# Performance work log

Measured on AMD Instinct MI355X. Metric: run time of the kernel, lower is better.

The kernel has to match this reference:

```python
import jax, jax.numpy as jnp
import numpy as np

B, S, H = 2, 1024, 1024
NH, NKV, HD = 16, 4, 64
F = 2816
E, K = 8, 2
WIN = 256
EPS = 1e-5
THETA = 10000.0


def setup_inputs() -> dict:
    key = jax.random.key(0)
    ks = jax.random.split(key, 13)
    n = lambda k, shp, s=0.02: jax.random.normal(k, shp, jnp.float32) * s
    return dict(
        hidden_states=jax.random.normal(ks[0], (B, S, H), jnp.float32),
        ln1_w=jnp.ones((H,), jnp.float32),
        q_w=n(ks[1], (H, NH * HD)),
        k_w=n(ks[2], (H, NKV * HD)),
        v_w=n(ks[3], (H, NKV * HD)),
        o_w=n(ks[4], (NH * HD, H)),
        res_ln_w=jnp.ones((H,), jnp.float32),
        rw1=n(ks[5], (H, H)),
        rw3=n(ks[6], (H, H)),
        rw2=n(ks[7], (H, H)),
        post_ln_w=jnp.ones((H,), jnp.float32),
        gate_w=n(ks[8], (H, E)),
        e_w1=n(ks[9], (E, H, F)),
        e_w3=n(ks[10], (E, H, F)),
        e_w2=n(ks[11], (E, F, H)),
    )


def _rms(x, w):
    v = jnp.mean(jnp.square(x), -1, keepdims=True)
    return x * jax.lax.rsqrt(v + EPS) * w


def _rope(x):
    # x: [B,S,h,HD]; standard rotate-half RoPE
    pos = jnp.arange(S, dtype=jnp.float32)
    inv = 1.0 / (THETA ** (jnp.arange(0, HD, 2, dtype=jnp.float32) / HD))
    ang = pos[:, None] * inv  # [S, HD/2]
    cos = jnp.concatenate([jnp.cos(ang)] * 2, -1)[None, :, None, :]
    sin = jnp.concatenate([jnp.sin(ang)] * 2, -1)[None, :, None, :]
    x1, x2 = jnp.split(x, 2, axis=-1)
    rot = jnp.concatenate([-x2, x1], -1)
    return x * cos + rot * sin


def _attn(x, q_w, k_w, v_w, o_w):
    q = (x @ q_w).reshape(B, S, NH, HD)
    k = (x @ k_w).reshape(B, S, NKV, HD)
    v = (x @ v_w).reshape(B, S, NKV, HD)
    q, k = _rope(q), _rope(k)
    rep = NH // NKV
    k = jnp.repeat(k, rep, axis=2)
    v = jnp.repeat(v, rep, axis=2)
    sc = jnp.einsum('bqhd,bkhd->bhqk', q, k) * (HD ** -0.5)
    qi = jnp.arange(S)[:, None]
    ki = jnp.arange(S)[None, :]
    mask = (ki <= qi) & (qi - ki < WIN)  # causal sliding window
    sc = jnp.where(mask[None, None], sc, jnp.finfo(sc.dtype).min)
    p = jax.nn.softmax(sc, -1)
    o = jnp.einsum('bhqk,bkhd->bqhd', p, v).reshape(B, S, NH * HD)
    return o @ o_w


def _mlp(x, w1, w3, w2):
    return (jax.nn.silu(x @ w1) * (x @ w3)) @ w2


def _moe(x, gate_w, w1, w3, w2):
    xf = x.reshape(-1, H)  # [T,H]
    T = xf.shape[0]
    logits = xf @ gate_w
    probs = jax.nn.softmax(logits.astype(jnp.float32), -1)
    tw, ti = jax.lax.top_k(probs, K)
    tw = tw / jnp.sum(tw, -1, keepdims=True)
    # combine weights [T,E] via scatter of top-k weights
    cw = jnp.zeros((T, E), jnp.float32).at[jnp.arange(T)[:, None], ti].add(tw)
    h = jax.nn.silu(jnp.einsum('th,ehf->etf', xf, w1)) * jnp.einsum('th,ehf->etf', xf, w3)
    y = jnp.einsum('etf,efh->eth', h, w2)
    out = jnp.einsum('te,eth->th', cw, y)
    return out.reshape(B, S, H)


def reference(hidden_states, ln1_w, q_w, k_w, v_w, o_w, res_ln_w, rw1, rw3, rw2,
              post_ln_w, gate_w, e_w1, e_w3, e_w2):
    residual_input = hidden_states
    h = _rms(hidden_states, ln1_w)
    h = _attn(h, q_w, k_w, v_w, o_w)
    residual_attn = residual_input + h
    # parallel residual dense MLP path (is_residual_mlp=True -> ffn_dim=hidden)
    h = _rms(residual_attn, res_ln_w)
    h = _mlp(h, rw1, rw3, rw2)
    residual_residual = residual_attn + h
    # sparse MoE path operates on the ORIGINAL layer input (Arctic parallel path)
    h = _rms(residual_input, post_ln_w)
    h = _moe(h, gate_w, e_w1, e_w3, e_w2)
    return residual_residual + h
```

## Files before the change

### kernel.cpp

```cpp
#include <hip/hip_runtime.h>
#include <hip/hip_bf16.h>
#include <math.h>

#define B_    2
#define S_    1024
#define H_    1024
#define NH_   16
#define NKV_  4
#define HD_   64
#define F_    2816
#define E_    8
#define WIN_  256
#define T_    (B_*S_)
#define EPS_  1e-5f
#define QKVN_ 1536

typedef __hip_bfloat16 bf16;
using f32x4  = __attribute__((ext_vector_type(4))) float;
using bf16x8 = __attribute__((ext_vector_type(8))) short;

__device__ __forceinline__ float silu_f(float x) { return x / (1.0f + expf(-x)); }

__device__ __forceinline__ unsigned short f2bf(float v) {
  __hip_bfloat16 b = __float2bfloat16(v);
  return *reinterpret_cast<unsigned short*>(&b);
}

__device__ __forceinline__ void stage16(const void* g, void* l) {
#if defined(__has_builtin) && __has_builtin(__builtin_amdgcn_global_load_lds)
  __builtin_amdgcn_global_load_lds((const __attribute__((address_space(1))) unsigned int*)g,
                                   (__attribute__((address_space(3))) unsigned int*)l,
                                   16, 0, 0);
#else
  *(float4*)l = *(const float4*)g;
#endif
}

__global__ void rope_table_kernel(float* __restrict__ costab, float* __restrict__ sintab,
                                  int* __restrict__ counts) {
  int idx = blockIdx.x * blockDim.x + threadIdx.x;
  if (blockIdx.x == 0 && threadIdx.x < E_) counts[threadIdx.x] = 0;
  if (idx >= S_ * 32) return;
  int s = idx >> 5, j = idx & 31;
  float inv = powf(10000.0f, -(float)j / 32.0f);
  float ang = (float)s * inv;
  costab[idx] = cosf(ang);
  sintab[idx] = sinf(ang);
}

__global__ void transpose_cvt_kernel(const float* __restrict__ src, bf16* __restrict__ dst,
                                     int K, int N) {
  __shared__ float tile[32][33];
  const size_t bstride = (size_t)K * N;
  src += bstride * blockIdx.z;
  dst += bstride * blockIdx.z;
  int bk = blockIdx.x * 32, bn = blockIdx.y * 32;
  int tx = threadIdx.x & 31, ty = threadIdx.x >> 5;
  #pragma unroll
  for (int i = 0; i < 4; ++i)
    tile[ty + i * 8][tx] = src[(size_t)(bk + ty + i * 8) * N + bn + tx];
  __syncthreads();
  #pragma unroll
  for (int i = 0; i < 4; ++i)
    dst[(size_t)(bn + ty + i * 8) * K + bk + tx] = __float2bfloat16(tile[tx][ty + i * 8]);
}

struct TransBatch { const float* src[5]; bf16* dst[5]; };
__global__ void transpose_cvt5_kernel(TransBatch tb, int K, int N) {
  __shared__ float tile[32][33];
  const float* src = tb.src[blockIdx.z];
  bf16* dst = tb.dst[blockIdx.z];
  int bk = blockIdx.x * 32, bn = blockIdx.y * 32;
  int tx = threadIdx.x & 31, ty = threadIdx.x >> 5;
  #pragma unroll
  for (int i = 0; i < 4; ++i)
    tile[ty + i * 8][tx] = src[(size_t)(bk + ty + i * 8) * N + bn + tx];
  __syncthreads();
  #pragma unroll
  for (int i = 0; i < 4; ++i)
    dst[(size_t)(bn + ty + i * 8) * K + bk + tx] = __float2bfloat16(tile[tx][ty + i * 8]);
}

__global__ void rms_kernel(const float* __restrict__ x, const float* __restrict__ w,
                           bf16* __restrict__ ob) {
  const int row = blockIdx.x, t = threadIdx.x;
  const float* xr = x + (size_t)row * H_;
  float4 v = *(const float4*)(&xr[t * 4]);
  float ss = v.x*v.x + v.y*v.y + v.z*v.z + v.w*v.w;
  #pragma unroll
  for (int o = 32; o > 0; o >>= 1) ss += __shfl_xor(ss, o);
  __shared__ float red[4];
  if ((t & 63) == 0) red[t >> 6] = ss;
  __syncthreads();
  float tot = red[0] + red[1] + red[2] + red[3];
  float scale = rsqrtf(tot * (1.0f / H_) + EPS_);
  float4 wv = *(const float4*)(&w[t * 4]);
  ushort4 pk = { f2bf(v.x*scale*wv.x), f2bf(v.y*scale*wv.y),
                 f2bf(v.z*scale*wv.z), f2bf(v.w*scale*wv.w) };
  *(ushort4*)((unsigned short*)ob + (size_t)row * H_ + t * 4) = pk;
}

__global__ void rms_gate_kernel(const float* __restrict__ x, const float* __restrict__ w,
                                const float* __restrict__ gw, bf16* __restrict__ ob,
                                int* __restrict__ counts, int* __restrict__ entries,
                                float* __restrict__ wgt) {
  const int row = blockIdx.x, t = threadIdx.x;
  const float* xr = x + (size_t)row * H_;
  float4 v = *(const float4*)(&xr[t * 4]);
  float ss = v.x*v.x + v.y*v.y + v.z*v.z + v.w*v.w;
  #pragma unroll
  for (int o = 32; o > 0; o >>= 1) ss += __shfl_xor(ss, o);
  __shared__ float red[4];
  __shared__ float sm[4][8];
  if ((t & 63) == 0) red[t >> 6] = ss;
  __syncthreads();
  float tot = red[0] + red[1] + red[2] + red[3];
  float scale = rsqrtf(tot * (1.0f / H_) + EPS_);
  float4 wv = *(const float4*)(&w[t * 4]);
  float o0 = v.x*scale*wv.x, o1 = v.y*scale*wv.y, o2 = v.z*scale*wv.z, o3 = v.w*scale*wv.w;
  ushort4 pk = { f2bf(o0), f2bf(o1), f2bf(o2), f2bf(o3) };
  *(ushort4*)((unsigned short*)ob + (size_t)row * H_ + t * 4) = pk;
  const float* gr = gw + (size_t)(t * 4) * E_;
  float acc[E_];
  #pragma unroll
  for (int e = 0; e < E_; ++e)
    acc[e] = o0 * gr[e] + o1 * gr[E_ + e] + o2 * gr[2 * E_ + e] + o3 * gr[3 * E_ + e];
  #pragma unroll
  for (int e = 0; e < E_; ++e) {
    #pragma unroll
    for (int o = 32; o > 0; o >>= 1) acc[e] += __shfl_xor(acc[e], o);
  }
  if ((t & 63) == 0) {
    #pragma unroll
    for (int e = 0; e < E_; ++e) sm[t >> 6][e] = acc[e];
  }
  __syncthreads();
  if (t == 0) {
    float lg[E_];
    #pragma unroll
    for (int e = 0; e < E_; ++e) lg[e] = sm[0][e] + sm[1][e] + sm[2][e] + sm[3][e];
    float m = lg[0];
    #pragma unroll
    for (int e = 1; e < E_; ++e) m = fmaxf(m, lg[e]);
    float p[E_];
    #pragma unroll
    for (int e = 0; e < E_; ++e) p[e] = expf(lg[e] - m);
    int i0 = 0; float b0 = p[0];
    #pragma unroll
    for (int e = 1; e < E_; ++e) if (p[e] > b0) { b0 = p[e]; i0 = e; }
    int i1 = -1; float b1 = -1.f;
    #pragma unroll
    for (int e = 0; e < E_; ++e) if (e != i0 && p[e] > b1) { b1 = p[e]; i1 = e; }
    float inv = 1.f / (b0 + b1);
    wgt[row * 2 + 0] = b0 * inv;
    wgt[row * 2 + 1] = b1 * inv;
    int pos0 = atomicAdd(&counts[i0], 1);
    entries[i0 * T_ + pos0] = row * 2 + 0;
    int pos1 = atomicAdd(&counts[i1], 1);
    entries[i1 * T_ + pos1] = row * 2 + 1;
  }
}

template <int BN, bool ADD_RES>
__global__ __launch_bounds__(256)
void mm_kernel(const bf16* __restrict__ A, const bf16* __restrict__ Bt,
               const float* __restrict__ Res, float* __restrict__ C,
               int M, int N, int K) {
  __shared__ char Al[2][8192];
  __shared__ char Bl[2][BN * 64];
  const int t = threadIdx.x;
  const int m0 = blockIdx.y * 128, n0 = blockIdx.x * BN;
  const int lane = t & 63, wid = t >> 6;
  const int wr = wid >> 1, wc = wid & 1;
  const int sr = t >> 2, sc = t & 3;
  const int cA0 = sc ^ ((sr >> 1) & 3);
  const int cA1 = sc ^ (((sr + 64) >> 1) & 3);
  const bf16* gA0 = A + (size_t)(m0 + sr) * K + cA0 * 8;
  const bf16* gA1 = A + (size_t)(m0 + sr + 64) * K + cA1 * 8;
  const bf16* gB0 = Bt + (size_t)(n0 + sr) * K + cA0 * 8;
  const bf16* gB1 = Bt + (size_t)(n0 + sr + 64) * K + cA1 * 8;
  const int la = lane & 15, kg = lane >> 4;
  const int swz = (kg ^ ((la >> 1) & 3)) * 16;
  const int aoff = (wr * 64 + la) * 64 + swz;
  constexpr int NW = BN / 32;
  const int boff = (wc * (BN / 2) + la) * 64 + swz;
  auto STAGE = [&](int buf, int k0) {
    stage16(gA0 + k0, Al[buf] + t * 16);
    stage16(gA1 + k0, Al[buf] + 4096 + t * 16);
    stage16(gB0 + k0, Bl[buf] + t * 16);
    if constexpr (BN == 128) stage16(gB1 + k0, Bl[buf] + 4096 + t * 16);
  };
  f32x4 acc[4][NW] = {};
  STAGE(0, 0);
  __syncthreads();
  for (int k0 = 0; k0 < K; k0 += 32) {
    const int cur = (k0 >> 5) & 1;
    if (k0 + 32 < K) STAGE(cur ^ 1, k0 + 32);
    bf16x8 af[4], bfr[NW];
    #pragma unroll
    for (int i = 0; i < 4; ++i) af[i] = *(const bf16x8*)(Al[cur] + aoff + i * 1024);
    #pragma unroll
    for (int i = 0; i < NW; ++i) bfr[i] = *(const bf16x8*)(Bl[cur] + boff + i * 1024);
    #pragma unroll
    for (int mi = 0; mi < 4; ++mi)
      #pragma unroll
      for (int ni = 0; ni < NW; ++ni)
        acc[mi][ni] = __builtin_amdgcn_mfma_f32_16x16x32_bf16(af[mi], bfr[ni], acc[mi][ni], 0, 0, 0);
    __syncthreads();
  }
  #pragma unroll
  for (int mi = 0; mi < 4; ++mi) {
    int row = m0 + wr * 64 + mi * 16 + kg * 4;
    #pragma unroll
    for (int ni = 0; ni < NW; ++ni) {
      int col = n0 + wc * (BN / 2) + ni * 16 + la;
      #pragma unroll
      for (int r = 0; r < 4; ++r) {
        size_t off = (size_t)(row + r) * N + col;
        float v = acc[mi][ni][r];
        if (ADD_RES) v += Res[off];
        C[off] = v;
      }
    }
  }
}

__global__ void rope_cvt_qk_kernel(const float* __restrict__ QKV, const float* __restrict__ ct,
                                   const float* __restrict__ st, bf16* __restrict__ Qb,
                                   bf16* __restrict__ Kb) {
  int idx = blockIdx.x * 256 + threadIdx.x;
  int j = idx & 31;
  int hh = (idx >> 5) % 20;
  int t = idx / (32 * 20);
  int s = t & (S_ - 1), b = t >> 10;
  float c = ct[s * 32 + j], sn = st[s * 32 + j];
  if (hh < NH_) {
    const float* src = QKV + (size_t)t * QKVN_ + hh * HD_;
    float x1 = src[j], x2 = src[j + 32];
    bf16* dst = Qb + ((size_t)(b * NH_ + hh) * S_ + s) * HD_;
    dst[j]      = __float2bfloat16((x1 * c - x2 * sn) * 0.125f);
    dst[j + 32] = __float2bfloat16((x2 * c + x1 * sn) * 0.125f);
  } else {
    int kvh = hh - NH_;
    const float* src = QKV + (size_t)t * QKVN_ + 1024 + kvh * HD_;
    float x1 = src[j], x2 = src[j + 32];
    bf16* dst = Kb + ((size_t)(b * NKV_ + kvh) * S_ + s) * HD_;
    dst[j]      = __float2bfloat16(x1 * c - x2 * sn);
    dst[j + 32] = __float2bfloat16(x2 * c + x1 * sn);
  }
}

__global__ void vt_kernel(const float* __restrict__ QKV, bf16* __restrict__ Vt) {
  int p = blockIdx.z;
  int b = p >> 2, kvh = p & 3;
  int s0 = blockIdx.x * 32, d0 = blockIdx.y * 32;
  __shared__ float tile[32][33];
  int tx = threadIdx.x & 31, ty = threadIdx.x >> 5;
  const float* src = QKV + (size_t)(b * S_) * QKVN_ + 1280 + kvh * HD_;
  #pragma unroll
  for (int i = 0; i < 4; ++i)
    tile[ty + i * 8][tx] = src[(size_t)(s0 + ty + i * 8) * QKVN_ + d0 + tx];
  __syncthreads();
  bf16* dst = Vt + (size_t)p * HD_ * S_;
  #pragma unroll
  for (int i = 0; i < 4; ++i)
    dst[(size_t)(d0 + ty + i * 8) * S_ + s0 + tx] = __float2bfloat16(tile[tx][ty + i * 8]);
}

__global__ __launch_bounds__(256)
void attn_kernel(const bf16* __restrict__ Qb, const bf16* __restrict__ Kb,
                 const bf16* __restrict__ Vt, bf16* __restrict__ O) {
  const int w = threadIdx.x >> 6, lane = threadIdx.x & 63;
  const int qw = blockIdx.x * 64 + w * 16;
  const int h = blockIdx.y, b = blockIdx.z, kvh = h >> 2;
  const int g = lane >> 4, qcol = lane & 15;
  const bf16* Qp = Qb + ((size_t)(b * NH_ + h) * S_ + qw) * HD_;
  const bf16* Kp = Kb + (size_t)(b * NKV_ + kvh) * S_ * HD_;
  const bf16* Vp = Vt + (size_t)(b * NKV_ + kvh) * HD_ * S_;
  const bf16x8 qf0 = *(const bf16x8*)(Qp + qcol * HD_ + g * 8);
  const bf16x8 qf1 = *(const bf16x8*)(Qp + qcol * HD_ + 32 + g * 8);
  const int q = qw + qcol;
  float m = -3.0e38f, lsum = 0.f;
  f32x4 o[4] = {};
  int kstart = qw - (WIN_ - 1); if (kstart < 0) kstart = 0; kstart &= ~31;
  const int kend = qw + 16;
  for (int kt = kstart; kt < kend; kt += 32) {
    f32x4 s0 = {}, s1 = {};
    {
      const bf16* kr0 = Kp + (size_t)(kt + qcol) * HD_ + g * 8;
      const bf16* kr1 = kr0 + 16 * HD_;
      bf16x8 kf;
      kf = *(const bf16x8*)(kr0);      s0 = __builtin_amdgcn_mfma_f32_16x16x32_bf16(kf, qf0, s0, 0, 0, 0);
      kf = *(const bf16x8*)(kr0 + 32); s0 = __builtin_amdgcn_mfma_f32_16x16x32_bf16(kf, qf1, s0, 0, 0, 0);
      kf = *(const bf16x8*)(kr1);      s1 = __builtin_amdgcn_mfma_f32_16x16x32_bf16(kf, qf0, s1, 0, 0, 0);
      kf = *(const bf16x8*)(kr1 + 32); s1 = __builtin_amdgcn_mfma_f32_16x16x32_bf16(kf, qf1, s1, 0, 0, 0);
    }
    bool v0[4], v1[4];
    float pmax = -3.0e38f;
    #pragma unroll
    for (int r = 0; r < 4; ++r) {
      int k0r = kt + 4 * g + r;
      int k1r = k0r + 16;
      v0[r] = (k0r <= q) && (q - k0r < WIN_);
      v1[r] = (k1r <= q) && (q - k1r < WIN_);
      s0[r] = v0[r] ? s0[r] : -3.0e38f;
      s1[r] = v1[r] ? s1[r] : -3.0e38f;
      pmax = fmaxf(pmax, fmaxf(s0[r], s1[r]));
    }
    pmax = fmaxf(pmax, __shfl_xor(pmax, 16));
    pmax = fmaxf(pmax, __shfl_xor(pmax, 32));
    const float mnew = fmaxf(m, pmax);
    const float scale = __expf(m - mnew);
    float p0[4], p1[4], psum = 0.f;
    #pragma unroll
    for (int r = 0; r < 4; ++r) {
      p0[r] = v0[r] ? __expf(s0[r] - mnew) : 0.f;
      p1[r] = v1[r] ? __expf(s1[r] - mnew) : 0.f;
      psum += p0[r] + p1[r];
    }
    lsum = lsum * scale + psum;
    #pragma unroll
    for (int df = 0; df < 4; ++df) {
      o[df][0] *= scale; o[df][1] *= scale; o[df][2] *= scale; o[df][3] *= scale;
    }
    m = mnew;
    unsigned pk[4];
    #pragma unroll
    for (int r = 0; r < 4; ++r) pk[r] = (unsigned)f2bf(p0[r]) | ((unsigned)f2bf(p1[r]) << 16);
    const int srcLo = ((g & 1) << 1) * 16 + qcol;
    unsigned lo[4], hi[4];
    #pragma unroll
    for (int r = 0; r < 4; ++r) {
      lo[r] = (unsigned)__shfl((int)pk[r], srcLo);
      hi[r] = (unsigned)__shfl((int)pk[r], srcLo + 16);
    }
    const bool useHi = (g >= 2);
    union { unsigned u[4]; bf16x8 v; } bp;
    {
      unsigned e0 = useHi ? (lo[0] >> 16) : (lo[0] & 0xffffu);
      unsigned e1 = useHi ? (lo[1] >> 16) : (lo[1] & 0xffffu);
      unsigned e2 = useHi ? (lo[2] >> 16) : (lo[2] & 0xffffu);
      unsigned e3 = useHi ? (lo[3] >> 16) : (lo[3] & 0xffffu);
      unsigned e4 = useHi ? (hi[0] >> 16) : (hi[0] & 0xffffu);
      unsigned e5 = useHi ? (hi[1] >> 16) : (hi[1] & 0xffffu);
      unsigned e6 = useHi ? (hi[2] >> 16) : (hi[2] & 0xffffu);
      unsigned e7 = useHi ? (hi[3] >> 16) : (hi[3] & 0xffffu);
      bp.u[0] = e0 | (e1 << 16);
      bp.u[1] = e2 | (e3 << 16);
      bp.u[2] = e4 | (e5 << 16);
      bp.u[3] = e6 | (e7 << 16);
    }
    #pragma unroll
    for (int df = 0; df < 4; ++df) {
      bf16x8 vf = *(const bf16x8*)(Vp + (size_t)(16 * df + qcol) * S_ + kt + g * 8);
      o[df] = __builtin_amdgcn_mfma_f32_16x16x32_bf16(vf, bp.v, o[df], 0, 0, 0);
    }
  }
  lsum += __shfl_xor(lsum, 16);
  lsum += __shfl_xor(lsum, 32);
  const float inv = 1.f / lsum;
  bf16* Op = O + (size_t)(b * S_ + q) * (NH_ * HD_) + h * HD_;
  #pragma unroll
  for (int df = 0; df < 4; ++df) {
    ushort4 st = { f2bf(o[df][0] * inv), f2bf(o[df][1] * inv),
                   f2bf(o[df][2] * inv), f2bf(o[df][3] * inv) };
    *(ushort4*)((unsigned short*)Op + 16 * df + 4 * g) = st;
  }
}

__global__ void silu_mul_kernel(const float* __restrict__ GU, unsigned short* __restrict__ out) {
  int idx = blockIdx.x * 256 + threadIdx.x;
  int tok = idx >> 8, c = idx & 255;
  const float4 gv = *(const float4*)(GU + (size_t)tok * 2048 + c * 4);
  const float4 uv = *(const float4*)(GU + (size_t)tok * 2048 + 1024 + c * 4);
  ushort4 pk = { f2bf(silu_f(gv.x) * uv.x), f2bf(silu_f(gv.y) * uv.y),
                 f2bf(silu_f(gv.z) * uv.z), f2bf(silu_f(gv.w) * uv.w) };
  *(ushort4*)(out + (size_t)tok * 1024 + c * 4) = pk;
}

__global__ __launch_bounds__(256)
void moe_ffn1_kernel(const bf16* __restrict__ X, const bf16* __restrict__ W1t,
                     const bf16* __restrict__ W3t,
                     const int* __restrict__ counts, const int* __restrict__ entries,
                     bf16* __restrict__ Hb) {
  const int e = blockIdx.z;
  const int n_e = counts[e];
  const int r0 = blockIdx.y * 128;
  if (r0 >= n_e) return;
  const int f0 = blockIdx.x * 128;
  __shared__ char Al[2][8192], B1l[2][8192], B3l[2][8192];
  __shared__ int rowent[128];
  const int t = threadIdx.x;
  if (t < 128) { int r = r0 + t; rowent[t] = (r < n_e) ? entries[e * T_ + r] : -1; }
  __syncthreads();
  const int lane = t & 63, wid = t >> 6, wr = wid >> 1, wc = wid & 1;
  const int sr = t >> 2, sc = t & 3;
  const int c0 = sc ^ ((sr >> 1) & 3);
  const int c1 = sc ^ (((sr + 64) >> 1) & 3);
  int ea = rowent[sr], eb = rowent[sr + 64];
  const bf16* gA0 = X + (size_t)(ea < 0 ? 0 : (ea >> 1)) * H_ + c0 * 8;
  const bf16* gA1 = X + (size_t)(eb < 0 ? 0 : (eb >> 1)) * H_ + c1 * 8;
  const bf16* W1b = W1t + (size_t)e * F_ * H_;
  const bf16* W3b = W3t + (size_t)e * F_ * H_;
  const bf16* gB10 = W1b + (size_t)(f0 + sr) * H_ + c0 * 8;
  const bf16* gB11 = W1b + (size_t)(f0 + sr + 64) * H_ + c1 * 8;
  const bf16* gB30 = W3b + (size_t)(f0 + sr) * H_ + c0 * 8;
  const bf16* gB31 = W3b + (size_t)(f0 + sr + 64) * H_ + c1 * 8;
  const int la = lane & 15, kg = lane >> 4;
  const int swz = (kg ^ ((la >> 1) & 3)) * 16;
  const int aoff = (wr * 64 + la) * 64 + swz;
  const int boff = (wc * 64 + la) * 64 + swz;
  auto STAGE = [&](int buf, int k0) {
    stage16(gA0 + k0, Al[buf] + t * 16);
    stage16(gA1 + k0, Al[buf] + 4096 + t * 16);
    stage16(gB10 + k0, B1l[buf] + t * 16);
    stage16(gB11 + k0, B1l[buf] + 4096 + t * 16);
    stage16(gB30 + k0, B3l[buf] + t * 16);
    stage16(gB31 + k0, B3l[buf] + 4096 + t * 16);
  };
  f32x4 acc1[4][4] = {}, acc3[4][4] = {};
  STAGE(0, 0);
  __syncthreads();
  for (int k0 = 0; k0 < H_; k0 += 32) {
    const int cur = (k0 >> 5) & 1;
    if (k0 + 32 < H_) STAGE(cur ^ 1, k0 + 32);
    bf16x8 af[4], b1f[4], b3f[4];
    #pragma unroll
    for (int i = 0; i < 4; ++i) af[i] = *(const bf16x8*)(Al[cur] + aoff + i * 1024);
    #pragma unroll
    for (int i = 0; i < 4; ++i) b1f[i] = *(const bf16x8*)(B1l[cur] + boff + i * 1024);
    #pragma unroll
    for (int i = 0; i < 4; ++i) b3f[i] = *(const bf16x8*)(B3l[cur] + boff + i * 1024);
    #pragma unroll
    for (int mi = 0; mi < 4; ++mi)
      #pragma unroll
      for (int ni = 0; ni < 4; ++ni) {
        acc1[mi][ni] = __builtin_amdgcn_mfma_f32_16x16x32_bf16(af[mi], b1f[ni], acc1[mi][ni], 0, 0, 0);
        acc3[mi][ni] = __builtin_amdgcn_mfma_f32_16x16x32_bf16(af[mi], b3f[ni], acc3[mi][ni], 0, 0, 0);
      }
    __syncthreads();
  }
  #pragma unroll
  for (int mi = 0; mi < 4; ++mi) {
    int rloc = wr * 64 + mi * 16 + kg * 4;
    #pragma unroll
    for (int ni = 0; ni < 4; ++ni) {
      int col = f0 + wc * 64 + ni * 16 + la;
      #pragma unroll
      for (int r = 0; r < 4; ++r) {
        int ent = rowent[rloc + r];
        if (ent < 0) continue;
        float gv = acc1[mi][ni][r], uv = acc3[mi][ni][r];
        Hb[(size_t)ent * F_ + col] = __float2bfloat16(silu_f(gv) * uv);
      }
    }
  }
}

__global__ __launch_bounds__(256)
void moe_ffn2_kernel(const bf16* __restrict__ Hb, const bf16* __restrict__ W2t,
                     const int* __restrict__ counts, const int* __restrict__ entries,
                     float* __restrict__ Y) {
  const int e = blockIdx.z;
  const int n_e = counts[e];
  const int r0 = blockIdx.y * 128;
  if (r0 >= n_e) return;
  const int n0 = blockIdx.x * 128;
  __shared__ char Al[2][8192], Bl[2][8192];
  __shared__ int rowent[128];
  const int t = threadIdx.x;
  if (t < 128) { int r = r0 + t; rowent[t] = (r < n_e) ? entries[e * T_ + r] : -1; }
  __syncthreads();
  const int lane = t & 63, wid = t >> 6, wr = wid >> 1, wc = wid & 1;
  const int sr = t >> 2, sc = t & 3;
  const int c0 = sc ^ ((sr >> 1) & 3);
  const int c1 = sc ^ (((sr + 64) >> 1) & 3);
  int ea = rowent[sr], eb = rowent[sr + 64];
  const bf16* gA0 = Hb + (size_t)(ea < 0 ? 0 : ea) * F_ + c0 * 8;
  const bf16* gA1 = Hb + (size_t)(eb < 0 ? 0 : eb) * F_ + c1 * 8;
  const bf16* W2b = W2t + (size_t)e * H_ * F_;
  const bf16* gB0 = W2b + (size_t)(n0 + sr) * F_ + c0 * 8;
  const bf16* gB1 = W2b + (size_t)(n0 + sr + 64) * F_ + c1 * 8;
  const int la = lane & 15, kg = lane >> 4;
  const int swz = (kg ^ ((la >> 1) & 3)) * 16;
  const int aoff = (wr * 64 + la) * 64 + swz;
  const int boff = (wc * 64 + la) * 64 + swz;
  auto STAGE = [&](int buf, int k0) {
    stage16(gA0 + k0, Al[buf] + t * 16);
    stage16(gA1 + k0, Al[buf] + 4096 + t * 16);
    stage16(gB0 + k0, Bl[buf] + t * 16);
    stage16(gB1 + k0, Bl[buf] + 4096 + t * 16);
  };
  f32x4 acc[4][4] = {};
  STAGE(0, 0);
  __syncthreads();
  for (int k0 = 0; k0 < F_; k0 += 32) {
    const int cur = (k0 >> 5) & 1;
    if (k0 + 32 < F_) STAGE(cur ^ 1, k0 + 32);
    bf16x8 af[4], bfr[4];
    #pragma unroll
    for (int i = 0; i < 4; ++i) af[i] = *(const bf16x8*)(Al[cur] + aoff + i * 1024);
    #pragma unroll
    for (int i = 0; i < 4; ++i) bfr[i] = *(const bf16x8*)(Bl[cur] + boff + i * 1024);
    #pragma unroll
    for (int mi = 0; mi < 4; ++mi)
      #pragma unroll
      for (int ni = 0; ni < 4; ++ni)
        acc[mi][ni] = __builtin_amdgcn_mfma_f32_16x16x32_bf16(af[mi], bfr[ni], acc[mi][ni], 0, 0, 0);
    __syncthreads();
  }
  #pragma unroll
  for (int mi = 0; mi < 4; ++mi) {
    int rloc = wr * 64 + mi * 16 + kg * 4;
    #pragma unroll
    for (int ni = 0; ni < 4; ++ni) {
      int col = n0 + wc * 64 + ni * 16 + la;
      #pragma unroll
      for (int r = 0; r < 4; ++r) {
        int ent = rowent[rloc + r];
        if (ent < 0) continue;
        Y[(size_t)ent * H_ + col] = acc[mi][ni][r];
      }
    }
  }
}

__global__ void combine_kernel(const float* __restrict__ Y, const float* __restrict__ wgt,
                               float* __restrict__ out) {
  int t = blockIdx.x;
  int c = threadIdx.x;
  float w0 = wgt[t * 2], w1 = wgt[t * 2 + 1];
  float4 y0 = *(const float4*)(&Y[((size_t)t * 2) * H_ + c * 4]);
  float4 y1 = *(const float4*)(&Y[((size_t)t * 2 + 1) * H_ + c * 4]);
  float4 o  = *(float4*)(&out[(size_t)t * H_ + c * 4]);
  o.x += w0 * y0.x + w1 * y1.x;
  o.y += w0 * y0.y + w1 * y1.y;
  o.z += w0 * y0.z + w1 * y1.z;
  o.w += w0 * y0.w + w1 * y1.w;
  *(float4*)(&out[(size_t)t * H_ + c * 4]) = o;
}

extern "C" void kernel_launch(void* const* d_in, const int* in_sizes, int n_in,
                              void* d_out, int out_size, void* d_ws, size_t ws_size,
                              hipStream_t stream) {
  const float* hidden    = (const float*)d_in[0];
  const float* ln1_w     = (const float*)d_in[1];
  const float* q_w       = (const float*)d_in[2];
  const float* k_w       = (const float*)d_in[3];
  const float* v_w       = (const float*)d_in[4];
  const float* o_w       = (const float*)d_in[5];
  const float* res_ln_w  = (const float*)d_in[6];
  const float* rw1       = (const float*)d_in[7];
  const float* rw3       = (const float*)d_in[8];
  const float* rw2       = (const float*)d_in[9];
  const float* post_ln_w = (const float*)d_in[10];
  const float* gate_w    = (const float*)d_in[11];
  const float* e_w1      = (const float*)d_in[12];
  const float* e_w3      = (const float*)d_in[13];
  const float* e_w2      = (const float*)d_in[14];
  float* out = (float*)d_out;

  char* base = (char*)d_ws;
  size_t off = 0;
  auto alloc = [&](size_t bytes) -> void* {
    void* p = base + off;
    off += (bytes + 255) & ~(size_t)255;
    return p;
  };
  float* qkvf   = (float*)alloc((size_t)T_ * QKVN_ * 4);
  float* costab = (float*)alloc((size_t)S_ * 32 * 4);
  float* sintab = (float*)alloc((size_t)S_ * 32 * 4);
  float* resat  = (float*)alloc((size_t)T_ * H_ * 4);
  float* gu     = (float*)alloc((size_t)T_ * 2048 * 4);
  float* wgt    = (float*)alloc((size_t)T_ * 2 * 4);
  float* Y      = (float*)alloc((size_t)T_ * 2 * H_ * 4);
  bf16* h1b     = (bf16*)alloc((size_t)T_ * H_ * 2);
  bf16* h2b     = (bf16*)alloc((size_t)T_ * H_ * 2);
  bf16* h3b     = (bf16*)alloc((size_t)T_ * H_ * 2);
  bf16* attnb   = (bf16*)alloc((size_t)T_ * H_ * 2);
  bf16* gb      = (bf16*)alloc((size_t)T_ * H_ * 2);
  bf16* Hb      = (bf16*)alloc((size_t)T_ * 2 * F_ * 2);
  bf16* Qbuf    = (bf16*)alloc((size_t)B_ * NH_ * S_ * HD_ * 2);
  bf16* Kbuf    = (bf16*)alloc((size_t)B_ * NKV_ * S_ * HD_ * 2);
  bf16* Vtbuf   = (bf16*)alloc((size_t)B_ * NKV_ * HD_ * S_ * 2);
  bf16* qkvwt   = (bf16*)alloc((size_t)QKVN_ * H_ * 2);
  bf16* owt     = (bf16*)alloc((size_t)H_ * H_ * 2);
  bf16* w13t    = (bf16*)alloc((size_t)2048 * H_ * 2);
  bf16* rw2t    = (bf16*)alloc((size_t)H_ * H_ * 2);
  bf16* ew1t    = (bf16*)alloc((size_t)E_ * F_ * H_ * 2);
  bf16* ew3t    = (bf16*)alloc((size_t)E_ * F_ * H_ * 2);
  bf16* ew2t    = (bf16*)alloc((size_t)E_ * H_ * F_ * 2);
  int* counts   = (int*)alloc(64);
  int* entries  = (int*)alloc((size_t)E_ * T_ * 4);

  rope_table_kernel<<<(S_ * 32 + 255) / 256, 256, 0, stream>>>(costab, sintab, counts);

  {
    TransBatch tb;
    tb.src[0] = q_w;  tb.dst[0] = qkvwt;
    tb.src[1] = o_w;  tb.dst[1] = owt;
    tb.src[2] = rw1;  tb.dst[2] = w13t;
    tb.src[3] = rw3;  tb.dst[3] = w13t + (size_t)1024 * 1024;
    tb.src[4] = rw2;  tb.dst[4] = rw2t;
    transpose_cvt5_kernel<<<dim3(32, 32, 5), 256, 0, stream>>>(tb, 1024, 1024);
  }
  {
    TransBatch tb = {};
    tb.src[0] = k_w;  tb.dst[0] = qkvwt + (size_t)1024 * 1024;
    tb.src[1] = v_w;  tb.dst[1] = qkvwt + (size_t)1280 * 1024;
    transpose_cvt5_kernel<<<dim3(32, 8, 2), 256, 0, stream>>>(tb, 1024, 256);
  }
  transpose_cvt_kernel<<<dim3(32, 88, 8), 256, 0, stream>>>(e_w1, ew1t, 1024, 2816);
  transpose_cvt_kernel<<<dim3(32, 88, 8), 256, 0, stream>>>(e_w3, ew3t, 1024, 2816);
  transpose_cvt_kernel<<<dim3(88, 32, 8), 256, 0, stream>>>(e_w2, ew2t, 2816, 1024);

  rms_kernel<<<T_, 256, 0, stream>>>(hidden, ln1_w, h1b);
  mm_kernel<64, false><<<dim3(QKVN_ / 64, T_ / 128), 256, 0, stream>>>(h1b, qkvwt, nullptr, qkvf, T_, QKVN_, H_);
  rope_cvt_qk_kernel<<<(T_ * 20 * 32) / 256, 256, 0, stream>>>(qkvf, costab, sintab, Qbuf, Kbuf);
  vt_kernel<<<dim3(32, 2, 8), 256, 0, stream>>>(qkvf, Vtbuf);
  attn_kernel<<<dim3(S_ / 64, NH_, B_), 256, 0, stream>>>(Qbuf, Kbuf, Vtbuf, attnb);
  mm_kernel<64, true><<<dim3(16, 16), 256, 0, stream>>>(attnb, owt, hidden, resat, T_, H_, H_);

  rms_kernel<<<T_, 256, 0, stream>>>(resat, res_ln_w, h2b);
  mm_kernel<128, false><<<dim3(16, 16), 256, 0, stream>>>(h2b, w13t, nullptr, gu, T_, 2048, H_);
  silu_mul_kernel<<<T_, 256, 0, stream>>>(gu, (unsigned short*)gb);
  mm_kernel<64, true><<<dim3(16, 16), 256, 0, stream>>>(gb, rw2t, resat, out, T_, H_, H_);

  rms_gate_kernel<<<T_, 256, 0, stream>>>(hidden, post_ln_w, gate_w, h3b, counts, entries, wgt);
  moe_ffn1_kernel<<<dim3(F_ / 128, 16, E_), 256, 0, stream>>>(h3b, ew1t, ew3t, counts, entries, Hb);
  moe_ffn2_kernel<<<dim3(8, 16, E_), 256, 0, stream>>>(Hb, ew2t, counts, entries, Y);
  combine_kernel<<<T_, 256, 0, stream>>>(Y, wgt, out);
}
```

Baseline: 749.3 us.

## Fuse dense MLP gate/up with SiLU, halve MoE tile N, use vmcnt-based waits

Adds a fused mlp13 kernel that computes the gate and up projections together and applies SiLU*mul in the epilogue, which removes the fp32 gu buffer and the separate silu_mul kernel. The MoE ffn1 and ffn2 kernels move from 128-wide to 64-wide N tiles, doubling the grid so more workgroups are available when per-expert row counts are small. The GEMM loops replace __syncthreads with explicit s_waitcnt vmcnt(N) plus s_barrier so the prefetch of the next tile can stay in flight across the barrier. Smaller tiles lower arithmetic intensity and reload A more often, and the hand-counted vmcnt values depend on how stage16 issues its loads.

```diff
diff --git a/kernel.cpp b/kernel.cpp
--- a/kernel.cpp
+++ b/kernel.cpp
@@ -168,6 +168,7 @@
                int M, int N, int K) {
   __shared__ char Al[2][8192];
   __shared__ char Bl[2][BN * 64];
+  constexpr int NL = (BN == 128) ? 4 : 3;
   const int t = threadIdx.x;
   const int m0 = blockIdx.y * 128, n0 = blockIdx.x * BN;
   const int lane = t & 63, wid = t >> 6;
@@ -192,10 +193,15 @@
   };
   f32x4 acc[4][NW] = {};
   STAGE(0, 0);
-  __syncthreads();
   for (int k0 = 0; k0 < K; k0 += 32) {
     const int cur = (k0 >> 5) & 1;
-    if (k0 + 32 < K) STAGE(cur ^ 1, k0 + 32);
+    if (k0 + 32 < K) {
+      STAGE(cur ^ 1, k0 + 32);
+      asm volatile("s_waitcnt vmcnt(%0)" :: "n"(NL) : "memory");
+    } else {
+      asm volatile("s_waitcnt vmcnt(0)" ::: "memory");
+    }
+    __builtin_amdgcn_s_barrier();
     bf16x8 af[4], bfr[NW];
     #pragma unroll
     for (int i = 0; i < 4; ++i) af[i] = *(const bf16x8*)(Al[cur] + aoff + i * 1024);
@@ -206,7 +212,7 @@
       #pragma unroll
       for (int ni = 0; ni < NW; ++ni)
         acc[mi][ni] = __builtin_amdgcn_mfma_f32_16x16x32_bf16(af[mi], bfr[ni], acc[mi][ni], 0, 0, 0);
-    __syncthreads();
+    __builtin_amdgcn_s_barrier();
   }
   #pragma unroll
   for (int mi = 0; mi < 4; ++mi) {
@@ -221,6 +227,70 @@
         if (ADD_RES) v += Res[off];
         C[off] = v;
       }
+    }
+  }
+}
+
+__global__ __launch_bounds__(256)
+void mlp13_kernel(const bf16* __restrict__ X, const bf16* __restrict__ W13t,
+                  bf16* __restrict__ Out) {
+  const int m0 = blockIdx.y * 128, f0 = blockIdx.x * 64;
+  __shared__ char Al[2][8192], B1l[2][4096], B3l[2][4096];
+  const int t = threadIdx.x;
+  const int lane = t & 63, wid = t >> 6, wr = wid >> 1, wc = wid & 1;
+  const int sr = t >> 2, sc = t & 3;
+  const int c0 = sc ^ ((sr >> 1) & 3);
+  const int c1 = sc ^ (((sr + 64) >> 1) & 3);
+  const bf16* gA0 = X + (size_t)(m0 + sr) * H_ + c0 * 8;
+  const bf16* gA1 = X + (size_t)(m0 + sr + 64) * H_ + c1 * 8;
+  const bf16* gB1 = W13t + (size_t)(f0 + sr) * H_ + c0 * 8;
+  const bf16* gB3 = W13t + (size_t)(1024 + f0 + sr) * H_ + c0 * 8;
+  const int la = lane & 15, kg = lane >> 4;
+  const int swz = (kg ^ ((la >> 1) & 3)) * 16;
+  const int aoff = (wr * 64 + la) * 64 + swz;
+  const int boff = (wc * 32 + la) * 64 + swz;
+  auto STAGE = [&](int buf, int k0) {
+    stage16(gA0 + k0, Al[buf] + t * 16);
+    stage16(gA1 + k0, Al[buf] + 4096 + t * 16);
+    stage16(gB1 + k0, B1l[buf] + t * 16);
+    stage16(gB3 + k0, B3l[buf] + t * 16);
+  };
+  f32x4 acc1[4][2] = {}, acc3[4][2] = {};
+  STAGE(0, 0);
+  for (int k0 = 0; k0 < H_; k0 += 32) {
+    const int cur = (k0 >> 5) & 1;
+    if (k0 + 32 < H_) {
+      STAGE(cur ^ 1, k0 + 32);
+      asm volatile("s_waitcnt vmcnt(4)" ::: "memory");
+    } else {
+      asm volatile("s_waitcnt vmcnt(0)" ::: "memory");
+    }
+    __builtin_amdgcn_s_barrier();
+    bf16x8 af[4], b1f[2], b3f[2];
+    #pragma unroll
+    for (int i = 0; i < 4; ++i) af[i] = *(const bf16x8*)(Al[cur] + aoff + i * 1024);
+    #pragma unroll
+    for (int i = 0; i < 2; ++i) b1f[i] = *(const bf16x8*)(B1l[cur] + boff + i * 1024);
+    #pragma unroll
+    for (int i = 0; i < 2; ++i) b3f[i] = *(const bf16x8*)(B3l[cur] + boff + i * 1024);
+    #pragma unroll
+    for (int mi = 0; mi < 4; ++mi)
+      #pragma unroll
+      for (int ni = 0; ni < 2; ++ni) {
+        acc1[mi][ni] = __builtin_amdgcn_mfma_f32_16x16x32_bf16(af[mi], b1f[ni], acc1[mi][ni], 0, 0, 0);
+        acc3[mi][ni] = __builtin_amdgcn_mfma_f32_16x16x32_bf16(af[mi], b3f[ni], acc3[mi][ni], 0, 0, 0);
+      }
+    __builtin_amdgcn_s_barrier();
+  }
+  #pragma unroll
+  for (int mi = 0; mi < 4; ++mi) {
+    int row = m0 + wr * 64 + mi * 16 + kg * 4;
+    #pragma unroll
+    for (int ni = 0; ni < 2; ++ni) {
+      int col = f0 + wc * 32 + ni * 16 + la;
+      #pragma unroll
+      for (int r = 0; r < 4; ++r)
+        Out[(size_t)(row + r) * 1024 + col] = __float2bfloat16(silu_f(acc1[mi][ni][r]) * acc3[mi][ni][r]);
     }
   }
 }
@@ -368,16 +438,6 @@
   }
 }
 
-__global__ void silu_mul_kernel(const float* __restrict__ GU, unsigned short* __restrict__ out) {
-  int idx = blockIdx.x * 256 + threadIdx.x;
-  int tok = idx >> 8, c = idx & 255;
-  const float4 gv = *(const float4*)(GU + (size_t)tok * 2048 + c * 4);
-  const float4 uv = *(const float4*)(GU + (size_t)tok * 2048 + 1024 + c * 4);
-  ushort4 pk = { f2bf(silu_f(gv.x) * uv.x), f2bf(silu_f(gv.y) * uv.y),
-                 f2bf(silu_f(gv.z) * uv.z), f2bf(silu_f(gv.w) * uv.w) };
-  *(ushort4*)(out + (size_t)tok * 1024 + c * 4) = pk;
-}
-
 __global__ __launch_bounds__(256)
 void moe_ffn1_kernel(const bf16* __restrict__ X, const bf16* __restrict__ W1t,
                      const bf16* __restrict__ W3t,
@@ -387,8 +447,8 @@
   const int n_e = counts[e];
   const int r0 = blockIdx.y * 128;
   if (r0 >= n_e) return;
-  const int f0 = blockIdx.x * 128;
-  __shared__ char Al[2][8192], B1l[2][8192], B3l[2][8192];
+  const int f0 = blockIdx.x * 64;
+  __shared__ char Al[2][8192], B1l[2][4096], B3l[2][4096];
   __shared__ int rowent[128];
   const int t = threadIdx.x;
   if (t < 128) { int r = r0 + t; rowent[t] = (r < n_e) ? entries[e * T_ + r] : -1; }
@@ -402,50 +462,51 @@
   const bf16* gA1 = X + (size_t)(eb < 0 ? 0 : (eb >> 1)) * H_ + c1 * 8;
   const bf16* W1b = W1t + (size_t)e * F_ * H_;
   const bf16* W3b = W3t + (size_t)e * F_ * H_;
-  const bf16* gB10 = W1b + (size_t)(f0 + sr) * H_ + c0 * 8;
-  const bf16* gB11 = W1b + (size_t)(f0 + sr + 64) * H_ + c1 * 8;
-  const bf16* gB30 = W3b + (size_t)(f0 + sr) * H_ + c0 * 8;
-  const bf16* gB31 = W3b + (size_t)(f0 + sr + 64) * H_ + c1 * 8;
+  const bf16* gB1 = W1b + (size_t)(f0 + sr) * H_ + c0 * 8;
+  const bf16* gB3 = W3b + (size_t)(f0 + sr) * H_ + c0 * 8;
   const int la = lane & 15, kg = lane >> 4;
   const int swz = (kg ^ ((la >> 1) & 3)) * 16;
   const int aoff = (wr * 64 + la) * 64 + swz;
-  const int boff = (wc * 64 + la) * 64 + swz;
+  const int boff = (wc * 32 + la) * 64 + swz;
   auto STAGE = [&](int buf, int k0) {
     stage16(gA0 + k0, Al[buf] + t * 16);
     stage16(gA1 + k0, Al[buf] + 4096 + t * 16);
-    stage16(gB10 + k0, B1l[buf] + t * 16);
-    stage16(gB11 + k0, B1l[buf] + 4096 + t * 16);
-    stage16(gB30 + k0, B3l[buf] + t * 16);
-    stage16(gB31 + k0, B3l[buf] + 4096 + t * 16);
+    stage16(gB1 + k0, B1l[buf] + t * 16);
+    stage16(gB3 + k0, B3l[buf] + t * 16);
   };
-  f32x4 acc1[4][4] = {}, acc3[4][4] = {};
+  f32x4 acc1[4][2] = {}, acc3[4][2] = {};
   STAGE(0, 0);
-  __syncthreads();
   for (int k0 = 0; k0 < H_; k0 += 32) {
     const int cur = (k0 >> 5) & 1;
-    if (k0 + 32 < H_) STAGE(cur ^ 1, k0 + 32);
-    bf16x8 af[4], b1f[4], b3f[4];
+    if (k0 + 32 < H_) {
+      STAGE(cur ^ 1, k0 + 32);
+      asm volatile("s_waitcnt vmcnt(4)" ::: "memory");
+    } else {
+      asm volatile("s_waitcnt vmcnt(0)" ::: "memory");
+    }
+    __builtin_amdgcn_s_barrier();
+    bf16x8 af[4], b1f[2], b3f[2];
     #pragma unroll
     for (int i = 0; i < 4; ++i) af[i] = *(const bf16x8*)(Al[cur] + aoff + i * 1024);
     #pragma unroll
-    for (int i = 0; i < 4; ++i) b1f[i] = *(const bf16x8*)(B1l[cur] + boff + i * 1024);
-    #pragma unroll
-    for (int i = 0; i < 4; ++i) b3f[i] = *(const bf16x8*)(B3l[cur] + boff + i * 1024);
+    for (int i = 0; i < 2; ++i) b1f[i] = *(const bf16x8*)(B1l[cur] + boff + i * 1024);
+    #pragma unroll
+    for (int i = 0; i < 2; ++i) b3f[i] = *(const bf16x8*)(B3l[cur] + boff + i * 1024);
     #pragma unroll
     for (int mi = 0; mi < 4; ++mi)
       #pragma unroll
-      for (int ni = 0; ni < 4; ++ni) {
+      for (int ni = 0; ni < 2; ++ni) {
         acc1[mi][ni] = __builtin_amdgcn_mfma_f32_16x16x32_bf16(af[mi], b1f[ni], acc1[mi][ni], 0, 0, 0);
         acc3[mi][ni] = __builtin_amdgcn_mfma_f32_16x16x32_bf16(af[mi], b3f[ni], acc3[mi][ni], 0, 0, 0);
       }
-    __syncthreads();
+    __builtin_amdgcn_s_barrier();
   }
   #pragma unroll
   for (int mi = 0; mi < 4; ++mi) {
     int rloc = wr * 64 + mi * 16 + kg * 4;
     #pragma unroll
-    for (int ni = 0; ni < 4; ++ni) {
-      int col = f0 + wc * 64 + ni * 16 + la;
+    for (int ni = 0; ni < 2; ++ni) {
+      int col = f0 + wc * 32 + ni * 16 + la;
       #pragma unroll
       for (int r = 0; r < 4; ++r) {
         int ent = rowent[rloc + r];
@@ -465,8 +526,8 @@
   const int n_e = counts[e];
   const int r0 = blockIdx.y * 128;
   if (r0 >= n_e) return;
-  const int n0 = blockIdx.x * 128;
-  __shared__ char Al[2][8192], Bl[2][8192];
+  const int n0 = blockIdx.x * 64;
+  __shared__ char Al[2][8192], Bl[2][4096];
   __shared__ int rowent[128];
   const int t = threadIdx.x;
   if (t < 128) { int r = r0 + t; rowent[t] = (r < n_e) ? entries[e * T_ + r] : -1; }
@@ -480,41 +541,44 @@
   const bf16* gA1 = Hb + (size_t)(eb < 0 ? 0 : eb) * F_ + c1 * 8;
   const bf16* W2b = W2t + (size_t)e * H_ * F_;
   const bf16* gB0 = W2b + (size_t)(n0 + sr) * F_ + c0 * 8;
-  const bf16* gB1 = W2b + (size_t)(n0 + sr + 64) * F_ + c1 * 8;
   const int la = lane & 15, kg = lane >> 4;
   const int swz = (kg ^ ((la >> 1) & 3)) * 16;
   const int aoff = (wr * 64 + la) * 64 + swz;
-  const int boff = (wc * 64 + la) * 64 + swz;
+  const int boff = (wc * 32 + la) * 64 + swz;
   auto STAGE = [&](int buf, int k0) {
     stage16(gA0 + k0, Al[buf] + t * 16);
     stage16(gA1 + k0, Al[buf] + 4096 + t * 16);
     stage16(gB0 + k0, Bl[buf] + t * 16);
-    stage16(gB1 + k0, Bl[buf] + 4096 + t * 16);
   };
-  f32x4 acc[4][4] = {};
+  f32x4 acc[4][2] = {};
   STAGE(0, 0);
-  __syncthreads();
   for (int k0 = 0; k0 < F_; k0 += 32) {
     const int cur = (k0 >> 5) & 1;
-    if (k0 + 32 < F_) STAGE(cur ^ 1, k0 + 32);
-    bf16x8 af[4], bfr[4];
+    if (k0 + 32 < F_) {
+      STAGE(cur ^ 1, k0 + 32);
+      asm volatile("s_waitcnt vmcnt(3)" ::: "memory");
+    } else {
+      asm volatile("s_waitcnt vmcnt(0)" ::: "memory");
+    }
+    __builtin_amdgcn_s_barrier();
+    bf16x8 af[4], bfr[2];
     #pragma unroll
     for (int i = 0; i < 4; ++i) af[i] = *(const bf16x8*)(Al[cur] + aoff + i * 1024);
     #pragma unroll
-    for (int i = 0; i < 4; ++i) bfr[i] = *(const bf16x8*)(Bl[cur] + boff + i * 1024);
+    for (int i = 0; i < 2; ++i) bfr[i] = *(const bf16x8*)(Bl[cur] + boff + i * 1024);
     #pragma unroll
     for (int mi = 0; mi < 4; ++mi)
       #pragma unroll
-      for (int ni = 0; ni < 4; ++ni)
+      for (int ni = 0; ni < 2; ++ni)
         acc[mi][ni] = __builtin_amdgcn_mfma_f32_16x16x32_bf16(af[mi], bfr[ni], acc[mi][ni], 0, 0, 0);
-    __syncthreads();
+    __builtin_amdgcn_s_barrier();
   }
   #pragma unroll
   for (int mi = 0; mi < 4; ++mi) {
     int rloc = wr * 64 + mi * 16 + kg * 4;
     #pragma unroll
-    for (int ni = 0; ni < 4; ++ni) {
-      int col = n0 + wc * 64 + ni * 16 + la;
+    for (int ni = 0; ni < 2; ++ni) {
+      int col = n0 + wc * 32 + ni * 16 + la;
       #pragma unroll
       for (int r = 0; r < 4; ++r) {
         int ent = rowent[rloc + r];
@@ -571,7 +635,6 @@
   float* costab = (float*)alloc((size_t)S_ * 32 * 4);
   float* sintab = (float*)alloc((size_t)S_ * 32 * 4);
   float* resat  = (float*)alloc((size_t)T_ * H_ * 4);
-  float* gu     = (float*)alloc((size_t)T_ * 2048 * 4);
   float* wgt    = (float*)alloc((size_t)T_ * 2 * 4);
   float* Y      = (float*)alloc((size_t)T_ * 2 * H_ * 4);
   bf16* h1b     = (bf16*)alloc((size_t)T_ * H_ * 2);
@@ -622,12 +685,11 @@
   mm_kernel<64, true><<<dim3(16, 16), 256, 0, stream>>>(attnb, owt, hidden, resat, T_, H_, H_);
 
   rms_kernel<<<T_, 256, 0, stream>>>(resat, res_ln_w, h2b);
-  mm_kernel<128, false><<<dim3(16, 16), 256, 0, stream>>>(h2b, w13t, nullptr, gu, T_, 2048, H_);
-  silu_mul_kernel<<<T_, 256, 0, stream>>>(gu, (unsigned short*)gb);
+  mlp13_kernel<<<dim3(16, 16), 256, 0, stream>>>(h2b, w13t, gb);
   mm_kernel<64, true><<<dim3(16, 16), 256, 0, stream>>>(gb, rw2t, resat, out, T_, H_, H_);
 
   rms_gate_kernel<<<T_, 256, 0, stream>>>(hidden, post_ln_w, gate_w, h3b, counts, entries, wgt);
-  moe_ffn1_kernel<<<dim3(F_ / 128, 16, E_), 256, 0, stream>>>(h3b, ew1t, ew3t, counts, entries, Hb);
-  moe_ffn2_kernel<<<dim3(8, 16, E_), 256, 0, stream>>>(Hb, ew2t, counts, entries, Y);
+  moe_ffn1_kernel<<<dim3(F_ / 64, 16, E_), 256, 0, stream>>>(h3b, ew1t, ew3t, counts, entries, Hb);
+  moe_ffn2_kernel<<<dim3(H_ / 64, 16, E_), 256, 0, stream>>>(Hb, ew2t, counts, entries, Y);
   combine_kernel<<<T_, 256, 0, stream>>>(Y, wgt, out);
 }
```

New measurement: 703.3 us. 6.1% less time.
